# Kernel optimization log

Measured on AMD Instinct MI355X. Metric: run time of the kernel, lower is better.

## Reference

```python
import jax, jax.numpy as jnp
import numpy as np

B, L, D = 8, 4096, 1024


def setup_inputs() -> dict:
    key = jax.random.key(0)
    k1, k2, k3 = jax.random.split(key, 3)
    x = jax.random.normal(k1, (B, L, D), dtype=jnp.float32)
    # nn.Linear(d_model, d_model): weight [D, D] (out, in), bias [D]
    bound = 1.0 / np.sqrt(D)
    W = jax.random.uniform(k2, (D, D), dtype=jnp.float32, minval=-bound, maxval=bound)
    b = jax.random.uniform(k3, (D,), dtype=jnp.float32, minval=-bound, maxval=bound)
    return {"x": x, "W": W, "b": b}


def reference(x, W, b):
    # rfft then irfft with n = original length along the sequence dim.
    # (Mathematically the identity on real input, but we keep the ops to
    # match the original module's computation faithfully.)
    x_fft = jnp.fft.rfft(x, axis=1)                 # [B, L//2+1, D] complex64
    x_ifft = jnp.fft.irfft(x_fft, n=x.shape[1], axis=1)  # [B, L, D] float32
    # nn.Linear: y = x @ W^T + b
    return jnp.einsum('bld,ed->ble', x_ifft, W) + b
```

## Files before the change

kernel.cpp:

```cpp
#include <hip/hip_runtime.h>
#include <hip/hip_bf16.h>
#include <stdint.h>


typedef __bf16 bf16_t;
typedef __bf16 bf16x8 __attribute__((ext_vector_type(8)));
typedef float f32x4 __attribute__((ext_vector_type(4)));

typedef __attribute__((address_space(1))) const void gvoid;
typedef __attribute__((address_space(3))) void svoid;

__global__ __launch_bounds__(256) void cvt_frag_kernel(const float* __restrict__ in,
                                                       bf16_t* __restrict__ out,
                                                       int K, int ksh, long total8) {
  long tid = (long)blockIdx.x * 256 + threadIdx.x;
  if (tid >= total8) return;
  int lane = (int)(tid & 63);
  long s = tid >> 6;
  int kb = (int)(s & ((1 << ksh) - 1));
  long m16 = s >> ksh;
  long row = m16 * 16 + (lane & 15);
  int k0 = kb * 32 + (lane >> 4) * 8;
  const float* p = in + row * (long)K + k0;
  f32x4 v0 = *(const f32x4*)p;
  f32x4 v1 = *(const f32x4*)(p + 4);
  bf16x8 o;
  o[0] = (bf16_t)v0[0]; o[1] = (bf16_t)v0[1]; o[2] = (bf16_t)v0[2]; o[3] = (bf16_t)v0[3];
  o[4] = (bf16_t)v1[0]; o[5] = (bf16_t)v1[1]; o[6] = (bf16_t)v1[2]; o[7] = (bf16_t)v1[3];
  *(bf16x8*)(out + tid * 8) = o;
}


__device__ __forceinline__ void stage_half(const bf16_t* __restrict__ base, int tile16,
                                           int kdiv32, int t, int kb, int isB, int buf,
                                           bf16_t* lds, int wid, int lane8) {
#pragma unroll
  for (int r = 0; r < 2; ++r) {
    int s = r * 8 + wid;
    size_t gElem = ((((size_t)(tile16 + s)) * kdiv32 + (size_t)(t * 2 + kb)) << 9) + lane8;
    int dElem = buf * 32768 + isB * 16384 + (s * 2 + kb) * 512 + lane8;
    __builtin_amdgcn_global_load_lds((gvoid*)(base + gElem), (svoid*)(lds + dElem), 16, 0, 0);
  }
}

#define GATE6() asm volatile("s_waitcnt vmcnt(6)" ::: "memory")
#define BAR() __builtin_amdgcn_s_barrier()

__global__ __launch_bounds__(512, 2) void gemm8p_kernel(
    const bf16_t* __restrict__ A, const bf16_t* __restrict__ B,
    const float* __restrict__ bias, float* __restrict__ C,
    int M, int N, int K) {
  __shared__ __align__(16) bf16_t lds[65536];

  const int kdiv32 = K >> 5;
  const int NT = K >> 6;

  int nwg = gridDim.x;
  int bid = blockIdx.x;
  int wg = bid;
  if ((nwg & 7) == 0) wg = (bid & 7) * (nwg >> 3) + (bid >> 3);
  int ntn = N >> 8;
  int tm = wg / ntn, tn = wg % ntn;

  int tid = threadIdx.x;
  int wid = tid >> 6, lane = tid & 63;
  int wm = wid >> 2, wn = wid & 3;
  int qr = lane & 15, qg = lane >> 4;
  int lane8 = lane * 8;
  int wm8 = wm * 8;
  int wn4 = wn * 4;
  int tm16 = tm * 16, tn16 = tn * 16;

  f32x4 acc[8][4] = {};
  bf16x8 aF[8], bF[2];

#define STAGE_A(t, kb, buf) stage_half(A, tm16, kdiv32, (t), (kb), 0, (buf), lds, wid, lane8)
#define STAGE_B(t, kb, buf) stage_half(B, tn16, kdiv32, (t), (kb), 1, (buf), lds, wid, lane8)
#define LDA_(mm, kb, buf) (*(const bf16x8*)(lds + (buf)*32768 + ((wm8 + (mm)) * 2 + (kb)) * 512 + lane8))
#define LDB_(nn, kb, buf) (*(const bf16x8*)(lds + (buf)*32768 + 16384 + ((wn4 + (nn)) * 2 + (kb)) * 512 + lane8))

#define PHASE(buf, kb, nh, LOADA, STMT_STAGE, DO_GATE)                                     \
  do {                                                                                     \
    if (LOADA) {                                                                           \
      _Pragma("unroll") for (int m_ = 0; m_ < 8; ++m_) aF[m_] = LDA_(m_, kb, buf);         \
    }                                                                                      \
    bF[0] = LDB_(2 * (nh) + 0, kb, buf);                                                   \
    bF[1] = LDB_(2 * (nh) + 1, kb, buf);                                                   \
    STMT_STAGE;                                                                            \
    if (DO_GATE) GATE6();                                                                  \
    BAR();                                                                                 \
    __builtin_amdgcn_s_setprio(1);                                                         \
    _Pragma("unroll") for (int m_ = 0; m_ < 8; ++m_) {                                     \
      acc[m_][2 * (nh) + 0] = __builtin_amdgcn_mfma_f32_16x16x32_bf16(                     \
          aF[m_], bF[0], acc[m_][2 * (nh) + 0], 0, 0, 0);                                  \
      acc[m_][2 * (nh) + 1] = __builtin_amdgcn_mfma_f32_16x16x32_bf16(                     \
          aF[m_], bF[1], acc[m_][2 * (nh) + 1], 0, 0, 0);                                  \
    }                                                                                      \
    __builtin_amdgcn_s_setprio(0);                                                         \
    BAR();                                                                                 \
  } while (0)

  STAGE_A(0, 0, 0); STAGE_B(0, 0, 0); STAGE_A(0, 1, 0); STAGE_B(0, 1, 0);
  STAGE_A(1, 0, 1); STAGE_B(1, 0, 1); STAGE_A(1, 1, 1);
  GATE6();
  BAR();

  for (int i = 0; i < (NT >> 1); ++i) {
    int t1 = 2 * i + 1;
    int t2 = 2 * i + 2; if (t2 >= NT) t2 -= 2;
    int t3 = 2 * i + 3; if (t3 >= NT) t3 -= 2;
    PHASE(0, 0, 0, 1, STAGE_B(t1, 1, 1), 0);
    PHASE(0, 0, 1, 0, STAGE_A(t2, 0, 0), 0);
    PHASE(0, 1, 0, 1, STAGE_B(t2, 0, 0), 0);
    PHASE(0, 1, 1, 0, STAGE_A(t2, 1, 0), 1);
    PHASE(1, 0, 0, 1, STAGE_B(t2, 1, 0), 0);
    PHASE(1, 0, 1, 0, STAGE_A(t3, 0, 1), 0);
    PHASE(1, 1, 0, 1, STAGE_B(t3, 0, 1), 0);
    PHASE(1, 1, 1, 0, STAGE_A(t3, 1, 1), 1);
  }

  int col0 = tn * 256 + wn * 64;
  int row0 = tm * 256 + wm * 128;
  float bv[4];
#pragma unroll
  for (int n = 0; n < 4; ++n) bv[n] = bias[col0 + n * 16 + qr];
#pragma unroll
  for (int m = 0; m < 8; ++m) {
#pragma unroll
    for (int r = 0; r < 4; ++r) {
      float* cr = C + (size_t)(row0 + m * 16 + qg * 4 + r) * N;
#pragma unroll
      for (int n = 0; n < 4; ++n)
        cr[col0 + n * 16 + qr] = acc[m][n][r] + bv[n];
    }
  }
#undef PHASE
#undef STAGE_A
#undef STAGE_B
#undef LDA_
#undef LDB_
}

__global__ __launch_bounds__(256) void naive_kernel(const float* __restrict__ x,
                                                    const float* __restrict__ W,
                                                    const float* __restrict__ b,
                                                    float* __restrict__ out,
                                                    int M, int N, int K) {
  long idx = (long)blockIdx.x * 256 + threadIdx.x;
  if (idx >= (long)M * N) return;
  int m = (int)(idx / N), n = (int)(idx % N);
  const float* xr = x + (size_t)m * K;
  const float* wr = W + (size_t)n * K;
  float s = 0.f;
  for (int k = 0; k < K; ++k) s += xr[k] * wr[k];
  out[idx] = s + b[n];
}

extern "C" void kernel_launch(void* const* d_in, const int* in_sizes, int n_in,
                              void* d_out, int out_size, void* d_ws, size_t ws_size,
                              hipStream_t stream) {
  const float* x = (const float*)d_in[0];
  const float* W = (const float*)d_in[1];
  const float* b = (const float*)d_in[2];
  float* out = (float*)d_out;

  int D = in_sizes[2];
  int M = in_sizes[0] / D;
  int N = D, K = D;

  int kdiv32 = K >> 5;
  size_t need = (size_t)(4u << 20) + (size_t)M * (size_t)K * sizeof(bf16_t);
  bool fast = (ws_size >= need) && (M % 256 == 0) && (N % 256 == 0) && (K % 128 == 0) &&
              (K >= 128) && ((kdiv32 & (kdiv32 - 1)) == 0) && (in_sizes[1] == N * K);

  if (fast) {
    int ksh = 0;
    while ((1 << (ksh + 1)) <= kdiv32) ++ksh;

    bf16_t* Wb = (bf16_t*)d_ws;
    bf16_t* Xb = (bf16_t*)((char*)d_ws + (4u << 20));

    long tW = (long)N * K / 8;
    hipLaunchKernelGGL(cvt_frag_kernel, dim3((unsigned)((tW + 255) / 256)), dim3(256), 0, stream,
                       W, Wb, K, ksh, tW);
    long tX = (long)M * K / 8;
    hipLaunchKernelGGL(cvt_frag_kernel, dim3((unsigned)((tX + 255) / 256)), dim3(256), 0, stream,
                       x, Xb, K, ksh, tX);

    int nwg = (M / 256) * (N / 256);
    hipLaunchKernelGGL(gemm8p_kernel, dim3(nwg), dim3(512), 0, stream,
                       Xb, Wb, b, out, M, N, K);
  } else {
    long total = (long)M * N;
    hipLaunchKernelGGL(naive_kernel, dim3((int)((total + 255) / 256)), dim3(256), 0, stream,
                       x, W, b, out, M, N, K);
  }
}
```

Measured before the change: 119.0 us.

## Restructure GEMM main loop into four-phase schedule with one barrier per phase

```diff
diff --git a/kernel.cpp b/kernel.cpp
--- a/kernel.cpp
+++ b/kernel.cpp
@@ -43,10 +43,7 @@
   }
 }
 
-#define GATE6() asm volatile("s_waitcnt vmcnt(6)" ::: "memory")
-#define BAR() __builtin_amdgcn_s_barrier()
-
-__global__ __launch_bounds__(512, 2) void gemm8p_kernel(
+__global__ __launch_bounds__(512, 2) void gemm4p_kernel(
     const bf16_t* __restrict__ A, const bf16_t* __restrict__ B,
     const float* __restrict__ bias, float* __restrict__ C,
     int M, int N, int K) {
@@ -72,51 +69,49 @@
   int tm16 = tm * 16, tn16 = tn * 16;
 
   f32x4 acc[8][4] = {};
-  bf16x8 aF[8], bF[2];
+  bf16x8 aF[8], bF[4];
 
 #define STAGE_A(t, kb, buf) stage_half(A, tm16, kdiv32, (t), (kb), 0, (buf), lds, wid, lane8)
 #define STAGE_B(t, kb, buf) stage_half(B, tn16, kdiv32, (t), (kb), 1, (buf), lds, wid, lane8)
 #define LDA_(mm, kb, buf) (*(const bf16x8*)(lds + (buf)*32768 + ((wm8 + (mm)) * 2 + (kb)) * 512 + lane8))
 #define LDB_(nn, kb, buf) (*(const bf16x8*)(lds + (buf)*32768 + 16384 + ((wn4 + (nn)) * 2 + (kb)) * 512 + lane8))
 
-#define PHASE(buf, kb, nh, LOADA, STMT_STAGE, DO_GATE)                                     \
+#define PHASE(buf, kb, ts, kbs, sbuf, GN, DO_STAGE, DO_BAR)                                \
   do {                                                                                     \
-    if (LOADA) {                                                                           \
-      _Pragma("unroll") for (int m_ = 0; m_ < 8; ++m_) aF[m_] = LDA_(m_, kb, buf);         \
+    _Pragma("unroll") for (int m_ = 0; m_ < 8; ++m_) aF[m_] = LDA_(m_, kb, buf);           \
+    _Pragma("unroll") for (int n_ = 0; n_ < 4; ++n_) bF[n_] = LDB_(n_, kb, buf);           \
+    if (DO_STAGE) { STAGE_A((ts), (kbs), (sbuf)); STAGE_B((ts), (kbs), (sbuf)); }          \
+    __builtin_amdgcn_s_setprio(1);                                                         \
+    _Pragma("unroll") for (int m_ = 0; m_ < 8; ++m_)                                       \
+      _Pragma("unroll") for (int n_ = 0; n_ < 4; ++n_)                                     \
+        acc[m_][n_] = __builtin_amdgcn_mfma_f32_16x16x32_bf16(aF[m_], bF[n_],              \
+                                                              acc[m_][n_], 0, 0, 0);       \
+    __builtin_amdgcn_s_setprio(0);                                                         \
+    if (DO_BAR) {                                                                          \
+      asm volatile("s_waitcnt vmcnt(" #GN ")" ::: "memory");                               \
+      __builtin_amdgcn_s_barrier();                                                        \
     }                                                                                      \
-    bF[0] = LDB_(2 * (nh) + 0, kb, buf);                                                   \
-    bF[1] = LDB_(2 * (nh) + 1, kb, buf);                                                   \
-    STMT_STAGE;                                                                            \
-    if (DO_GATE) GATE6();                                                                  \
-    BAR();                                                                                 \
-    __builtin_amdgcn_s_setprio(1);                                                         \
-    _Pragma("unroll") for (int m_ = 0; m_ < 8; ++m_) {                                     \
-      acc[m_][2 * (nh) + 0] = __builtin_amdgcn_mfma_f32_16x16x32_bf16(                     \
-          aF[m_], bF[0], acc[m_][2 * (nh) + 0], 0, 0, 0);                                  \
-      acc[m_][2 * (nh) + 1] = __builtin_amdgcn_mfma_f32_16x16x32_bf16(                     \
-          aF[m_], bF[1], acc[m_][2 * (nh) + 1], 0, 0, 0);                                  \
-    }                                                                                      \
-    __builtin_amdgcn_s_setprio(0);                                                         \
-    BAR();                                                                                 \
   } while (0)
 
-  STAGE_A(0, 0, 0); STAGE_B(0, 0, 0); STAGE_A(0, 1, 0); STAGE_B(0, 1, 0);
-  STAGE_A(1, 0, 1); STAGE_B(1, 0, 1); STAGE_A(1, 1, 1);
-  GATE6();
-  BAR();
+  STAGE_A(0, 0, 0); STAGE_B(0, 0, 0);
+  STAGE_A(0, 1, 0); STAGE_B(0, 1, 0);
+  STAGE_A(1, 0, 1); STAGE_B(1, 0, 1);
+  asm volatile("s_waitcnt vmcnt(8)" ::: "memory");
+  __builtin_amdgcn_s_barrier();
 
-  for (int i = 0; i < (NT >> 1); ++i) {
-    int t1 = 2 * i + 1;
-    int t2 = 2 * i + 2; if (t2 >= NT) t2 -= 2;
-    int t3 = 2 * i + 3; if (t3 >= NT) t3 -= 2;
-    PHASE(0, 0, 0, 1, STAGE_B(t1, 1, 1), 0);
-    PHASE(0, 0, 1, 0, STAGE_A(t2, 0, 0), 0);
-    PHASE(0, 1, 0, 1, STAGE_B(t2, 0, 0), 0);
-    PHASE(0, 1, 1, 0, STAGE_A(t2, 1, 0), 1);
-    PHASE(1, 0, 0, 1, STAGE_B(t2, 1, 0), 0);
-    PHASE(1, 0, 1, 0, STAGE_A(t3, 0, 1), 0);
-    PHASE(1, 1, 0, 1, STAGE_B(t3, 0, 1), 0);
-    PHASE(1, 1, 1, 0, STAGE_A(t3, 1, 1), 1);
+  for (int i = 0; i < (NT >> 1) - 1; ++i) {
+    int t1 = 2 * i + 1, t2 = 2 * i + 2, t3 = 2 * i + 3;
+    PHASE(0, 0, t1, 1, 1, 8, 1, 1);
+    PHASE(0, 1, t2, 0, 0, 8, 1, 1);
+    PHASE(1, 0, t2, 1, 0, 8, 1, 1);
+    PHASE(1, 1, t3, 0, 1, 8, 1, 1);
+  }
+  {
+    int t1 = NT - 1;
+    PHASE(0, 0, t1, 1, 1, 8, 1, 1);
+    PHASE(0, 1, 0, 0, 0, 4, 0, 1);
+    PHASE(1, 0, 0, 0, 0, 0, 0, 1);
+    PHASE(1, 1, 0, 0, 0, 0, 0, 0);
   }
 
   int col0 = tn * 256 + wn * 64;
@@ -188,7 +183,7 @@
                        x, Xb, K, ksh, tX);
 
     int nwg = (M / 256) * (N / 256);
-    hipLaunchKernelGGL(gemm8p_kernel, dim3(nwg), dim3(512), 0, stream,
+    hipLaunchKernelGGL(gemm4p_kernel, dim3(nwg), dim3(512), 0, stream,
                        Xb, Wb, b, out, M, N, K);
   } else {
     long total = (long)M * N;
```

Measured after the change: 117.7 us. No clear change (-1.1%).
